# Kernel optimization log

Hardware: AMD Instinct MI355X
Metric: run time of the kernel (lower is better)

## Reference

```python
import jax, jax.numpy as jnp
import numpy as np

N_NODES = 100000
N_REL = 8
IN_FEATS = 64
ATTN_FEATS = 32
NUM_HEADS = 4
N_EDGES = 800000
NEG_SLOPE = 0.2


def setup_inputs() -> dict:
    key = jax.random.key(0)
    ks = jax.random.split(key, 11)
    s = 0.05
    return {
        "feat": jax.random.normal(ks[0], (N_NODES, IN_FEATS), jnp.float32),
        "quality_emb": jax.random.normal(ks[1], (N_NODES, IN_FEATS), jnp.float32),
        "fc_src_w": jax.random.normal(ks[2], (N_REL, IN_FEATS, ATTN_FEATS * NUM_HEADS), jnp.float32) * s,
        "fc_src_b": jax.random.normal(ks[3], (N_REL, ATTN_FEATS * NUM_HEADS), jnp.float32) * s,
        "fc_qual_w": jax.random.normal(ks[4], (N_REL, IN_FEATS, ATTN_FEATS * NUM_HEADS), jnp.float32) * s,
        "fc_qual_b": jax.random.normal(ks[5], (N_REL, ATTN_FEATS * NUM_HEADS), jnp.float32) * s,
        "attn": jax.random.normal(ks[6], (N_REL, NUM_HEADS, ATTN_FEATS), jnp.float32) * s,
        "src": jax.random.randint(ks[7], (N_EDGES,), 0, N_NODES, jnp.int64),
        "dst": jax.random.randint(ks[8], (N_EDGES,), 0, N_NODES, jnp.int64),
        "r_type": jax.random.randint(ks[9], (N_EDGES,), 0, N_REL, jnp.int64),
        "nid": jax.random.randint(ks[10], (N_EDGES,), 0, N_NODES, jnp.int64),
    }


def reference(feat, quality_emb, fc_src_w, fc_src_b, fc_qual_w, fc_qual_b, attn,
              src, dst, r_type, nid):
    # gather_mm(feat[src], fc_src_w, idx_b=r_type) == project per node for all
    # relations (grouped GEMM), then gather [src, r_type] per edge.
    feat_proj = jnp.einsum('ni,rio->nro', feat, fc_src_w)          # [N, R, H*D]
    el = feat_proj[src, r_type] + fc_src_b[r_type]                 # [E, H*D]

    qual_proj = jnp.einsum('ni,rio->nro', quality_emb, fc_qual_w)  # [N, R, H*D]
    qual = qual_proj[nid, r_type] + fc_qual_b[r_type]              # [E, H*D]

    e = jax.nn.leaky_relu((el + qual).reshape(-1, NUM_HEADS, ATTN_FEATS), NEG_SLOPE)
    score = jnp.sum(e * attn[r_type], axis=-1)                     # [E, H]

    # edge softmax grouped by destination node, per head
    m = jax.ops.segment_max(score, dst, num_segments=N_NODES)      # [N, H]
    p = jnp.exp(score - m[dst])
    denom = jax.ops.segment_sum(p, dst, num_segments=N_NODES)      # [N, H]
    a = p / denom[dst]                                             # [E, H]

    # narre: messages use raw source features, weighted by attention
    msg = feat[src][:, None, :] * a[:, :, None]                    # [E, H, IN]
    ft = jax.ops.segment_sum(msg, dst, num_segments=N_NODES)       # [N, H, IN]
    return ft
```

## Files before the change

### kernel.cpp

```cpp
#include <hip/hip_runtime.h>
#include <hip/hip_bf16.h>

#define RELS 8
#define HDD 128
#define NH 4
#define STILES 4

typedef __attribute__((ext_vector_type(8))) short bf16x8;
typedef __attribute__((ext_vector_type(4))) float f32x4;
typedef unsigned short u16;

__device__ __forceinline__ u16 f2b(float v){
  union { float f; unsigned u; } x; x.f = v;
  unsigned r = x.u + 0x7fffu + ((x.u >> 16) & 1u);
  return (u16)(r >> 16);
}
__device__ __forceinline__ float b2f(u16 h){
  union { unsigned u; float f; } x; x.u = ((unsigned)h) << 16; return x.f;
}

template<int CTRL>
__device__ __forceinline__ float dpp_mov(float x){
  union { float f; int i; } u; u.f = x;
  u.i = __builtin_amdgcn_update_dpp(0, u.i, CTRL, 0xF, 0xF, false);
  return u.f;
}
__device__ __forceinline__ float row_sum16(float v){
  v += dpp_mov<0x121>(v);
  v += dpp_mov<0x122>(v);
  v += dpp_mov<0x124>(v);
  v += dpp_mov<0x128>(v);
  return v;
}

__global__ void k_combo(const float* __restrict__ wsrc, const float* __restrict__ wqual,
                        const float* __restrict__ bsrc, const float* __restrict__ bqual,
                        u16* __restrict__ Wt, float* __restrict__ biasc,
                        const float* __restrict__ feat, const float* __restrict__ qual,
                        u16* __restrict__ featb, u16* __restrict__ qualb, int total,
                        const int* __restrict__ rt,
                        int* __restrict__ rcnt, int E,
                        int BH, int B0){
  int b = blockIdx.x, t = threadIdx.x;
  if (b < BH){
    __shared__ int lh[RELS];
    if (t < RELS) lh[t] = 0;
    __syncthreads();
    for (int e = b*256 + t; e < E; e += BH*256)
      atomicAdd(&lh[rt[e]], 1);
    __syncthreads();
    if (t < RELS && lh[t]) atomicAdd(&rcnt[t], lh[t]);
  } else if (b < BH + B0){
    int g = (b - BH)*256 + t;
    if (g < RELS*HDD*HDD){
      int r = g >> 14, rem = g & 16383, n = rem >> 7, k = rem & 127;
      float v = (k < 64) ? wsrc[r*8192 + k*128 + n] : wqual[r*8192 + (k-64)*128 + n];
      Wt[g] = f2b(v);
    } else {
      int bb = g - RELS*HDD*HDD;
      if (bb < RELS*HDD) biasc[bb] = bsrc[bb] + bqual[bb];
    }
  } else {
    int g = ((b - BH - B0)*256 + t) * 8;
    const float* sp; u16* dp;
    if (g < total){ sp = feat; dp = featb; }
    else { g -= total; if (g >= total) return; sp = qual; dp = qualb; }
    float4 a = *(const float4*)(sp + g);
    float4 c = *(const float4*)(sp + g + 4);
    union { u16 h[8]; uint4 v; } o;
    o.h[0]=f2b(a.x); o.h[1]=f2b(a.y); o.h[2]=f2b(a.z); o.h[3]=f2b(a.w);
    o.h[4]=f2b(c.x); o.h[5]=f2b(c.y); o.h[6]=f2b(c.z); o.h[7]=f2b(c.w);
    *(uint4*)(dp + g) = o.v;
  }
}

__global__ void k_scatter(const int* __restrict__ rt,
                          const int* __restrict__ src, const int* __restrict__ nid,
                          const int* __restrict__ dst,
                          const int* __restrict__ rcnt, int* __restrict__ rcur,
                          int* __restrict__ srcR, int* __restrict__ nidR,
                          int* __restrict__ dstR, int E){
  __shared__ int lh[RELS], lb[RELS];
  int t = threadIdx.x;
  if (t < RELS) lh[t] = 0;
  __syncthreads();
  int e = blockIdx.x*256 + t;
  int r = 0, rank = 0, sv = 0, nv = 0, dv = 0;
  if (e < E){
    sv = src[e]; nv = nid[e]; dv = dst[e];
    r = rt[e];
    rank = atomicAdd(&lh[r], 1);
  }
  __syncthreads();
  if (t < RELS){
    int ro = 0;
    #pragma unroll
    for (int i=0;i<RELS;i++) if (i < t) ro += rcnt[i];
    if (lh[t] > 0) lb[t] = ro + atomicAdd(&rcur[t], lh[t]);
  }
  __syncthreads();
  if (e < E){
    int pr = lb[r] + rank;
    srcR[pr] = sv;
    nidR[pr] = nv;
    dstR[pr] = dv;
  }
}

__global__ void k_scan_a(const int* __restrict__ deg, int* __restrict__ offD,
                         int* __restrict__ bsums, int N){
  __shared__ int s[256];
  int t = threadIdx.x, i = blockIdx.x*256 + t;
  int v = (i < N) ? deg[i] : 0;
  s[t] = v; __syncthreads();
  for (int off=1; off<256; off<<=1){
    int x = (t >= off) ? s[t-off] : 0;
    __syncthreads();
    s[t] += x;
    __syncthreads();
  }
  if (i < N) offD[i] = s[t] - v;
  if (t == 255) bsums[blockIdx.x] = s[255];
}

__global__ void k_scan_b(const int* __restrict__ bsums, int* __restrict__ bsums_sc,
                         int* __restrict__ offD, int NBLK, int N){
  __shared__ int s[512];
  int t = threadIdx.x;
  int v = (t < NBLK) ? bsums[t] : 0;
  s[t] = v; __syncthreads();
  for (int off=1; off<512; off<<=1){
    int x = (t >= off) ? s[t-off] : 0;
    __syncthreads();
    s[t] += x;
    __syncthreads();
  }
  if (t < NBLK) bsums_sc[t] = s[t] - v;
  if (t == NBLK-1) offD[N] = s[t];
}

__global__ void k_scan_c(int* __restrict__ offD, const int* __restrict__ bsums_sc, int N){
  int i = blockIdx.x*256 + threadIdx.x;
  if (i < N) offD[i] += bsums_sc[i >> 8];
}

__global__ __launch_bounds__(320) void k_score(
    const u16* __restrict__ featb, const u16* __restrict__ qualb,
    const u16* __restrict__ Wt, const float* __restrict__ biasc,
    const float* __restrict__ attn,
    const int* __restrict__ srcR, const int* __restrict__ nidR,
    const int* __restrict__ dstR, const int* __restrict__ rcnt,
    int* __restrict__ deg, int* __restrict__ rankR,
    float* __restrict__ scoreR, int E){
  __shared__ u16 As[2][64*128];
  int t = threadIdx.x;

  int bid = blockIdx.x;
  int r = -1, base = 0, cntR = 0;
  {
    int acc0 = 0, st = 0;
    #pragma unroll
    for (int rr=0; rr<RELS; rr++){
      int c = rcnt[rr];
      int nb = (c + 255) >> 8;
      if (r < 0 && bid < acc0 + nb){
        int ch = bid - acc0;
        r = rr; base = st + ch*256; cntR = min(256, c - ch*256);
      }
      acc0 += nb;
      st += c;
    }
  }
  if (r < 0) return;
  int Tact = (cntR + 63) >> 6;

  if (t >= 256){
    int hl = t - 256;
    int eh0=-1,eh1=-1,eh2=-1,eh3=-1;
    int rk0=0,rk1=0,rk2=0,rk3=0;
    if (hl < cntR)     { eh0 = base+hl;     rk0 = atomicAdd(&deg[dstR[eh0]],1); }
    if (64+hl < cntR)  { eh1 = base+64+hl;  rk1 = atomicAdd(&deg[dstR[eh1]],1); }
    if (128+hl < cntR) { eh2 = base+128+hl; rk2 = atomicAdd(&deg[dstR[eh2]],1); }
    if (192+hl < cntR) { eh3 = base+192+hl; rk3 = atomicAdd(&deg[dstR[eh3]],1); }
    for (int i=0;i<Tact;i++)
      __builtin_amdgcn_s_barrier();
    if (eh0>=0) rankR[eh0]=rk0;
    if (eh1>=0) rankR[eh1]=rk1;
    if (eh2>=0) rankR[eh2]=rk2;
    if (eh3>=0) rankR[eh3]=rk3;
    return;
  }

  int mloc = t >> 2, part = t & 3;
  int lane = t & 63, w = t >> 6;
  int lr = lane & 15, lq = lane >> 4;

  const u16* wbase = Wt + r*16384 + (w*32)*128;
  bf16x8 wfrag[2][4];
  #pragma unroll
  for (int mt=0; mt<2; mt++)
    #pragma unroll
    for (int kt=0; kt<4; kt++)
      wfrag[mt][kt] = *(const bf16x8*)(wbase + (mt*16 + lr)*128 + kt*32 + lq*8);

  float attn_p[2][4], attn_n[2][4];
  f32x4 biasv[2];
  #pragma unroll
  for (int mt=0; mt<2; mt++)
    #pragma unroll
    for (int i=0; i<4; i++){
      int c = w*32 + mt*16 + lq*4 + i;
      float a = attn[r*128 + c];
      biasv[mt][i] = biasc[r*128 + c];
      attn_p[mt][i] = a;
      attn_n[mt][i] = 0.2f*a;
    }

  const u16* basep = (part < 2) ? featb : qualb;
  int halfoff = (part & 1)*32;
  int myidx[STILES];
  #pragma unroll
  for (int tt=0; tt<STILES; tt++){
    int eloc = tt*64 + mloc;
    int gi = base + eloc;
    myidx[tt] = (eloc < cntR) ? ((part < 2) ? srcR[gi] : nidR[gi]) : -1;
  }

  uint4 pre[2][4];
  auto fetch = [&](int pb, int idxval){
    if (idxval >= 0){
      const uint4* pv = (const uint4*)(basep + (long long)idxval*64 + halfoff);
      pre[pb][0]=pv[0]; pre[pb][1]=pv[1]; pre[pb][2]=pv[2]; pre[pb][3]=pv[3];
    } else {
      uint4 z = {0,0,0,0};
      pre[pb][0]=z; pre[pb][1]=z; pre[pb][2]=z; pre[pb][3]=z;
    }
  };

  fetch(0, myidx[0]);
  fetch(1, myidx[1]);
  #pragma unroll
  for (int tt=0; tt<STILES; tt++){
    if (tt >= Tact) break;
    const int p = tt & 1;
    uint4* As_v = (uint4*)As[p];
    #pragma unroll
    for (int i=0;i<4;i++){
      int c = part*4 + i;
      As_v[mloc*16 + (c ^ part ^ (mloc & 7))] = pre[p][i];
    }
    if (tt+2 < STILES) fetch(p, myidx[tt+2]);
    asm volatile("s_waitcnt lgkmcnt(0)" ::: "memory");
    __builtin_amdgcn_s_barrier();

    f32x4 acc[4][2];
    #pragma unroll
    for (int et=0; et<4; et++){ acc[et][0]=biasv[0]; acc[et][1]=biasv[1]; }
    #pragma unroll
    for (int et=0; et<4; et++){
      #pragma unroll
      for (int kt=0; kt<4; kt++){
        bf16x8 bf = *(const bf16x8*)&As[p][(et*16 + lr)*128 + (((kt*4 + lq) ^ kt ^ (lr & 7))*8)];
        acc[et][0] = __builtin_amdgcn_mfma_f32_16x16x32_bf16(wfrag[0][kt], bf, acc[et][0], 0, 0, 0);
        acc[et][1] = __builtin_amdgcn_mfma_f32_16x16x32_bf16(wfrag[1][kt], bf, acc[et][1], 0, 0, 0);
      }
    }

    float s0v=0.f, s1v=0.f, s2v=0.f, s3v=0.f;
    #pragma unroll
    for (int mt=0; mt<2; mt++)
      #pragma unroll
      for (int i=0; i<4; i++){
        float x0 = acc[0][mt][i];
        s0v = __builtin_fmaf(fmaxf(x0,0.f), attn_p[mt][i], s0v);
        s0v = __builtin_fmaf(fminf(x0,0.f), attn_n[mt][i], s0v);
        float x1 = acc[1][mt][i];
        s1v = __builtin_fmaf(fmaxf(x1,0.f), attn_p[mt][i], s1v);
        s1v = __builtin_fmaf(fminf(x1,0.f), attn_n[mt][i], s1v);
        float x2 = acc[2][mt][i];
        s2v = __builtin_fmaf(fmaxf(x2,0.f), attn_p[mt][i], s2v);
        s2v = __builtin_fmaf(fminf(x2,0.f), attn_n[mt][i], s2v);
        float x3 = acc[3][mt][i];
        s3v = __builtin_fmaf(fmaxf(x3,0.f), attn_p[mt][i], s3v);
        s3v = __builtin_fmaf(fminf(x3,0.f), attn_n[mt][i], s3v);
      }
    s0v += __shfl_xor(s0v, 16); s0v += __shfl_xor(s0v, 32);
    s1v += __shfl_xor(s1v, 16); s1v += __shfl_xor(s1v, 32);
    s2v += __shfl_xor(s2v, 16); s2v += __shfl_xor(s2v, 32);
    s3v += __shfl_xor(s3v, 16); s3v += __shfl_xor(s3v, 32);
    float v01 = (lq & 1) ? s1v : s0v;
    float v23 = (lq & 1) ? s3v : s2v;
    float v = (lq & 2) ? v23 : v01;
    v = __expf(v);
    int eout = tt*64 + lane;
    if (eout < cntR) scoreR[(size_t)w*E + base + eout] = v;
  }
}

__global__ void k_perm(const int* __restrict__ dstR, const int* __restrict__ rankR,
                       const int* __restrict__ srcR, const float* __restrict__ scoreR,
                       const int* __restrict__ offD,
                       float* __restrict__ scoreD, int* __restrict__ srcD, int E){
  int pr = blockIdx.x*256 + threadIdx.x;
  if (pr >= E) return;
  int d = dstR[pr];
  int pd = offD[d] + rankR[pr];
  float4 sc;
  sc.x = scoreR[pr];
  sc.y = scoreR[(size_t)E + pr];
  sc.z = scoreR[(size_t)2*E + pr];
  sc.w = scoreR[(size_t)3*E + pr];
  *(float4*)&scoreD[(long long)pd*4] = sc;
  srcD[pd] = srcR[pr];
}

__global__ __launch_bounds__(256) void k_agg(
    const int* __restrict__ offD, const int* __restrict__ srcD,
    const float* __restrict__ scoreD,
    const u16* __restrict__ featb, float* __restrict__ out, int N){
  __shared__ float ps[4][64][4];
  __shared__ int   ss[4][64];
  int wv = threadIdx.x >> 6, lane = threadIdx.x & 63;
  int node = blockIdx.x*4 + wv;
  if (node >= N) return;
  int s0 = offD[node], s1 = offD[node+1];
  int deg = s1 - s0;
  float a0=0.f, a1=0.f, a2=0.f, a3=0.f;
  if (deg > 0){
    float d0=0.f,d1=0.f,d2=0.f,d3=0.f;
    for (int c=0; c<deg; c+=64){
      int j = c + lane;
      float p0=0.f,p1=0.f,p2=0.f,p3=0.f; int sv=0;
      if (j < deg){
        float4 sc = *(const float4*)&scoreD[(long long)(s0+j)*4];
        sv = srcD[s0+j];
        p0=sc.x; p1=sc.y; p2=sc.z; p3=sc.w;
      }
      d0+=p0; d1+=p1; d2+=p2; d3+=p3;
      float4 pv = { p0, p1, p2, p3 };
      *(float4*)&ps[wv][lane][0] = pv;
      ss[wv][lane] = sv;
      __builtin_amdgcn_wave_barrier();
      int cnt = min(64, deg - c);
      #pragma unroll 4
      for (int e=0; e<cnt; e++){
        float4 pe = *(const float4*)&ps[wv][e][0];
        float fv = b2f(featb[(long long)ss[wv][e]*64 + lane]);
        a0 += pe.x*fv; a1 += pe.y*fv; a2 += pe.z*fv; a3 += pe.w*fv;
      }
      __builtin_amdgcn_wave_barrier();
    }
    d0=row_sum16(d0); d1=row_sum16(d1); d2=row_sum16(d2); d3=row_sum16(d3);
    #pragma unroll
    for (int off=16; off<64; off<<=1){
      d0+=__shfl_xor(d0,off); d1+=__shfl_xor(d1,off);
      d2+=__shfl_xor(d2,off); d3+=__shfl_xor(d3,off);
    }
    a0 *= 1.f/d0; a1 *= 1.f/d1; a2 *= 1.f/d2; a3 *= 1.f/d3;
  }
  float* op = out + (long long)node*256;
  op[lane]       = a0;
  op[64 + lane]  = a1;
  op[128 + lane] = a2;
  op[192 + lane] = a3;
}

extern "C" void kernel_launch(void* const* d_in, const int* in_sizes, int n_in,
                              void* d_out, int out_size, void* d_ws, size_t ws_size,
                              hipStream_t stream) {
  const float* feat  = (const float*)d_in[0];
  const float* qual  = (const float*)d_in[1];
  const float* wsrc  = (const float*)d_in[2];
  const float* bsrc  = (const float*)d_in[3];
  const float* wqual = (const float*)d_in[4];
  const float* bqual = (const float*)d_in[5];
  const float* attn  = (const float*)d_in[6];
  const int* src = (const int*)d_in[7];
  const int* dst = (const int*)d_in[8];
  const int* rt  = (const int*)d_in[9];
  const int* nid = (const int*)d_in[10];
  const int E = in_sizes[7];
  const int N = in_sizes[0] / 64;
  float* out = (float*)d_out;

  char* p = (char*)d_ws;
  auto alloc = [&](size_t bytes) -> void* {
    void* q = (void*)p;
    p += (bytes + 255) & ~(size_t)255;
    return q;
  };
  float* scoreD  = (float*)alloc((size_t)E*4*4);
  float* scoreR  = (float*)alloc((size_t)E*4*4);
  u16*  featb    = (u16*)  alloc((size_t)N*64*2);
  u16*  qualb    = (u16*)  alloc((size_t)N*64*2);
  u16*  Wt       = (u16*)  alloc((size_t)RELS*HDD*HDD*2);
  float* biasc   = (float*)alloc((size_t)RELS*HDD*4);
  int*  srcD     = (int*)  alloc((size_t)E*4);
  int*  srcR     = (int*)  alloc((size_t)E*4);
  int*  nidR     = (int*)  alloc((size_t)E*4);
  int*  dstR     = (int*)  alloc((size_t)E*4);
  int*  rankR    = (int*)  alloc((size_t)E*4);
  int*  offD     = (int*)  alloc((size_t)(N+1)*4);
  int*  bsums    = (int*)  alloc(4096);
  int*  bsums_sc = (int*)  alloc(4096);
  char* zbase = p;
  int*  deg      = (int*)  alloc((size_t)N*4);
  int*  rcnt     = (int*)  alloc(32);
  int*  rcur     = (int*)  alloc(32);
  size_t zbytes = (size_t)(p - zbase);

  hipMemsetAsync(zbase, 0, zbytes, stream);

  int total = N*64;
  int totw = RELS*HDD*HDD + RELS*HDD;
  int BH = 512;
  int B0 = (totw + 255)/256;
  int B1 = ((2*total)/8 + 255)/256;
  int B2 = (E + 255)/256;
  k_combo<<<BH+B0+B1, 256, 0, stream>>>(wsrc, wqual, bsrc, bqual, Wt, biasc,
                                        feat, qual, featb, qualb, total,
                                        rt, rcnt, E, BH, B0);
  k_scatter<<<B2, 256, 0, stream>>>(rt, src, nid, dst, rcnt, rcur,
                                    srcR, nidR, dstR, E);
  int NBS = B2 + RELS;
  k_score<<<NBS, 320, 0, stream>>>(featb, qualb, Wt, biasc, attn,
                                   srcR, nidR, dstR, rcnt, deg, rankR, scoreR, E);
  int NBLK = (N + 255)/256;
  k_scan_a<<<NBLK, 256, 0, stream>>>(deg, offD, bsums, N);
  k_scan_b<<<1, 512, 0, stream>>>(bsums, bsums_sc, offD, NBLK, N);
  k_scan_c<<<NBLK, 256, 0, stream>>>(offD, bsums_sc, N);
  k_perm<<<B2, 256, 0, stream>>>(dstR, rankR, srcR, scoreR, offD, scoreD, srcD, E);
  k_agg<<<(N + 3)/4, 256, 0, stream>>>(offD, srcD, scoreD, featb, out, N);
}
```

Before: 370.1 us.

## Move degree counting into scatter and fuse permutation into score kernel

Destination-degree atomics and rank computation move from extra warps in the score kernel into the relation scatter kernel. The scan now runs before scoring, so the score kernel can write scores and source ids directly into destination-sorted order. This removes the separate permutation kernel and the intermediate relation-ordered score buffer. In exchange the score kernel does scattered 4-byte stores per head instead of a coalesced write, and it loses the overlap between the degree atomics and the MFMA work.

```diff
diff --git a/kernel.cpp b/kernel.cpp
--- a/kernel.cpp
+++ b/kernel.cpp
@@ -78,16 +78,18 @@
                           const int* __restrict__ src, const int* __restrict__ nid,
                           const int* __restrict__ dst,
                           const int* __restrict__ rcnt, int* __restrict__ rcur,
+                          int* __restrict__ deg,
                           int* __restrict__ srcR, int* __restrict__ nidR,
-                          int* __restrict__ dstR, int E){
+                          int* __restrict__ dstR, int* __restrict__ rankR, int E){
   __shared__ int lh[RELS], lb[RELS];
   int t = threadIdx.x;
   if (t < RELS) lh[t] = 0;
   __syncthreads();
   int e = blockIdx.x*256 + t;
-  int r = 0, rank = 0, sv = 0, nv = 0, dv = 0;
+  int r = 0, rank = 0, sv = 0, nv = 0, dv = 0, rk = 0;
   if (e < E){
     sv = src[e]; nv = nid[e]; dv = dst[e];
+    rk = atomicAdd(&deg[dv], 1);
     r = rt[e];
     rank = atomicAdd(&lh[r], 1);
   }
@@ -104,6 +106,7 @@
     srcR[pr] = sv;
     nidR[pr] = nv;
     dstR[pr] = dv;
+    rankR[pr] = rk;
   }
 }
 
@@ -144,15 +147,17 @@
   if (i < N) offD[i] += bsums_sc[i >> 8];
 }
 
-__global__ __launch_bounds__(320) void k_score(
+__global__ __launch_bounds__(256) void k_score(
     const u16* __restrict__ featb, const u16* __restrict__ qualb,
     const u16* __restrict__ Wt, const float* __restrict__ biasc,
     const float* __restrict__ attn,
     const int* __restrict__ srcR, const int* __restrict__ nidR,
-    const int* __restrict__ dstR, const int* __restrict__ rcnt,
-    int* __restrict__ deg, int* __restrict__ rankR,
-    float* __restrict__ scoreR, int E){
+    const int* __restrict__ dstR, const int* __restrict__ rankR,
+    const int* __restrict__ rcnt, const int* __restrict__ offD,
+    int* __restrict__ srcD,
+    float* __restrict__ scoreD){
   __shared__ u16 As[2][64*128];
+  __shared__ int pos_s[2][64];
   int t = threadIdx.x;
 
   int bid = blockIdx.x;
@@ -174,23 +179,6 @@
   if (r < 0) return;
   int Tact = (cntR + 63) >> 6;
 
-  if (t >= 256){
-    int hl = t - 256;
-    int eh0=-1,eh1=-1,eh2=-1,eh3=-1;
-    int rk0=0,rk1=0,rk2=0,rk3=0;
-    if (hl < cntR)     { eh0 = base+hl;     rk0 = atomicAdd(&deg[dstR[eh0]],1); }
-    if (64+hl < cntR)  { eh1 = base+64+hl;  rk1 = atomicAdd(&deg[dstR[eh1]],1); }
-    if (128+hl < cntR) { eh2 = base+128+hl; rk2 = atomicAdd(&deg[dstR[eh2]],1); }
-    if (192+hl < cntR) { eh3 = base+192+hl; rk3 = atomicAdd(&deg[dstR[eh3]],1); }
-    for (int i=0;i<Tact;i++)
-      __builtin_amdgcn_s_barrier();
-    if (eh0>=0) rankR[eh0]=rk0;
-    if (eh1>=0) rankR[eh1]=rk1;
-    if (eh2>=0) rankR[eh2]=rk2;
-    if (eh3>=0) rankR[eh3]=rk3;
-    return;
-  }
-
   int mloc = t >> 2, part = t & 3;
   int lane = t & 63, w = t >> 6;
   int lr = lane & 15, lq = lane >> 4;
@@ -218,12 +206,19 @@
 
   const u16* basep = (part < 2) ? featb : qualb;
   int halfoff = (part & 1)*32;
-  int myidx[STILES];
+  int myidx[STILES], mypos[STILES];
   #pragma unroll
   for (int tt=0; tt<STILES; tt++){
     int eloc = tt*64 + mloc;
+    bool v = (eloc < cntR);
     int gi = base + eloc;
-    myidx[tt] = (eloc < cntR) ? ((part < 2) ? srcR[gi] : nidR[gi]) : -1;
+    myidx[tt] = v ? ((part < 2) ? srcR[gi] : nidR[gi]) : -1;
+    mypos[tt] = -1;
+    if (part == 0 && v){
+      int pd = offD[dstR[gi]] + rankR[gi];
+      mypos[tt] = pd;
+      srcD[pd] = myidx[tt];
+    }
   }
 
   uint4 pre[2][4];
@@ -249,9 +244,9 @@
       int c = part*4 + i;
       As_v[mloc*16 + (c ^ part ^ (mloc & 7))] = pre[p][i];
     }
+    if (part == 0) pos_s[p][mloc] = mypos[tt];
     if (tt+2 < STILES) fetch(p, myidx[tt+2]);
-    asm volatile("s_waitcnt lgkmcnt(0)" ::: "memory");
-    __builtin_amdgcn_s_barrier();
+    __syncthreads();
 
     f32x4 acc[4][2];
     #pragma unroll
@@ -292,26 +287,9 @@
     float v23 = (lq & 1) ? s3v : s2v;
     float v = (lq & 2) ? v23 : v01;
     v = __expf(v);
-    int eout = tt*64 + lane;
-    if (eout < cntR) scoreR[(size_t)w*E + base + eout] = v;
-  }
-}
-
-__global__ void k_perm(const int* __restrict__ dstR, const int* __restrict__ rankR,
-                       const int* __restrict__ srcR, const float* __restrict__ scoreR,
-                       const int* __restrict__ offD,
-                       float* __restrict__ scoreD, int* __restrict__ srcD, int E){
-  int pr = blockIdx.x*256 + threadIdx.x;
-  if (pr >= E) return;
-  int d = dstR[pr];
-  int pd = offD[d] + rankR[pr];
-  float4 sc;
-  sc.x = scoreR[pr];
-  sc.y = scoreR[(size_t)E + pr];
-  sc.z = scoreR[(size_t)2*E + pr];
-  sc.w = scoreR[(size_t)3*E + pr];
-  *(float4*)&scoreD[(long long)pd*4] = sc;
-  srcD[pd] = srcR[pr];
+    int pd = pos_s[p][lane];
+    if (pd >= 0) scoreD[(long long)pd*4 + w] = v;
+  }
 }
 
 __global__ __launch_bounds__(256) void k_agg(
@@ -390,7 +368,6 @@
     return q;
   };
   float* scoreD  = (float*)alloc((size_t)E*4*4);
-  float* scoreR  = (float*)alloc((size_t)E*4*4);
   u16*  featb    = (u16*)  alloc((size_t)N*64*2);
   u16*  qualb    = (u16*)  alloc((size_t)N*64*2);
   u16*  Wt       = (u16*)  alloc((size_t)RELS*HDD*HDD*2);
@@ -420,15 +397,15 @@
   k_combo<<<BH+B0+B1, 256, 0, stream>>>(wsrc, wqual, bsrc, bqual, Wt, biasc,
                                         feat, qual, featb, qualb, total,
                                         rt, rcnt, E, BH, B0);
-  k_scatter<<<B2, 256, 0, stream>>>(rt, src, nid, dst, rcnt, rcur,
-                                    srcR, nidR, dstR, E);
-  int NBS = B2 + RELS;
-  k_score<<<NBS, 320, 0, stream>>>(featb, qualb, Wt, biasc, attn,
-                                   srcR, nidR, dstR, rcnt, deg, rankR, scoreR, E);
+  k_scatter<<<B2, 256, 0, stream>>>(rt, src, nid, dst, rcnt, rcur, deg,
+                                    srcR, nidR, dstR, rankR, E);
   int NBLK = (N + 255)/256;
   k_scan_a<<<NBLK, 256, 0, stream>>>(deg, offD, bsums, N);
   k_scan_b<<<1, 512, 0, stream>>>(bsums, bsums_sc, offD, NBLK, N);
   k_scan_c<<<NBLK, 256, 0, stream>>>(offD, bsums_sc, N);
-  k_perm<<<B2, 256, 0, stream>>>(dstR, rankR, srcR, scoreR, offD, scoreD, srcD, E);
+  int NBS = B2 + RELS;
+  k_score<<<NBS, 256, 0, stream>>>(featb, qualb, Wt, biasc, attn,
+                                   srcR, nidR, dstR, rankR, rcnt, offD,
+                                   srcD, scoreD);
   k_agg<<<(N + 3)/4, 256, 0, stream>>>(offD, srcD, scoreD, featb, out, N);
 }
```

New measurement: 335.7 us. 9.3% less time.

## Move degree histogram into dedicated blocks and pad degree counters

Applied to the files above, without the earlier changes.

The per-edge atomic degree counting moves out of the extra 64-thread wave in each score block and into 256 dedicated leading blocks that grid-stride over edges with four loads and atomics in flight per thread. Score blocks drop to 256 threads and no longer run the barrier-matching loop for the histogram wave. Each degree counter is padded to 16 ints so that concurrent atomics on different nodes do not hit the same cache line. The cost is a 16x larger zeroed degree array and strided reads in the scan.

```diff
diff --git a/kernel.cpp b/kernel.cpp
--- a/kernel.cpp
+++ b/kernel.cpp
@@ -5,6 +5,8 @@
 #define HDD 128
 #define NH 4
 #define STILES 4
+#define DEGS 16
+#define BHIST 256
 
 typedef __attribute__((ext_vector_type(8))) short bf16x8;
 typedef __attribute__((ext_vector_type(4))) float f32x4;
@@ -111,7 +113,7 @@
                          int* __restrict__ bsums, int N){
   __shared__ int s[256];
   int t = threadIdx.x, i = blockIdx.x*256 + t;
-  int v = (i < N) ? deg[i] : 0;
+  int v = (i < N) ? deg[(size_t)i*DEGS] : 0;
   s[t] = v; __syncthreads();
   for (int off=1; off<256; off<<=1){
     int x = (t >= off) ? s[t-off] : 0;
@@ -144,7 +146,7 @@
   if (i < N) offD[i] += bsums_sc[i >> 8];
 }
 
-__global__ __launch_bounds__(320) void k_score(
+__global__ __launch_bounds__(256) void k_score(
     const u16* __restrict__ featb, const u16* __restrict__ qualb,
     const u16* __restrict__ Wt, const float* __restrict__ biasc,
     const float* __restrict__ attn,
@@ -154,8 +156,25 @@
     float* __restrict__ scoreR, int E){
   __shared__ u16 As[2][64*128];
   int t = threadIdx.x;
-
-  int bid = blockIdx.x;
+  int b = blockIdx.x;
+
+  if (b < BHIST){
+    const int stride = BHIST*256;
+    for (int pr0 = b*256 + t; pr0 < E; pr0 += 4*stride){
+      int prs[4], dvs[4], rks[4];
+      #pragma unroll
+      for (int u=0;u<4;u++) prs[u] = pr0 + u*stride;
+      #pragma unroll
+      for (int u=0;u<4;u++) if (prs[u] < E) dvs[u] = dstR[prs[u]];
+      #pragma unroll
+      for (int u=0;u<4;u++) if (prs[u] < E) rks[u] = atomicAdd(&deg[(size_t)dvs[u]*DEGS], 1);
+      #pragma unroll
+      for (int u=0;u<4;u++) if (prs[u] < E) rankR[prs[u]] = rks[u];
+    }
+    return;
+  }
+
+  int bid = b - BHIST;
   int r = -1, base = 0, cntR = 0;
   {
     int acc0 = 0, st = 0;
@@ -173,23 +192,6 @@
   }
   if (r < 0) return;
   int Tact = (cntR + 63) >> 6;
-
-  if (t >= 256){
-    int hl = t - 256;
-    int eh0=-1,eh1=-1,eh2=-1,eh3=-1;
-    int rk0=0,rk1=0,rk2=0,rk3=0;
-    if (hl < cntR)     { eh0 = base+hl;     rk0 = atomicAdd(&deg[dstR[eh0]],1); }
-    if (64+hl < cntR)  { eh1 = base+64+hl;  rk1 = atomicAdd(&deg[dstR[eh1]],1); }
-    if (128+hl < cntR) { eh2 = base+128+hl; rk2 = atomicAdd(&deg[dstR[eh2]],1); }
-    if (192+hl < cntR) { eh3 = base+192+hl; rk3 = atomicAdd(&deg[dstR[eh3]],1); }
-    for (int i=0;i<Tact;i++)
-      __builtin_amdgcn_s_barrier();
-    if (eh0>=0) rankR[eh0]=rk0;
-    if (eh1>=0) rankR[eh1]=rk1;
-    if (eh2>=0) rankR[eh2]=rk2;
-    if (eh3>=0) rankR[eh3]=rk3;
-    return;
-  }
 
   int mloc = t >> 2, part = t & 3;
   int lane = t & 63, w = t >> 6;
@@ -404,7 +406,7 @@
   int*  bsums    = (int*)  alloc(4096);
   int*  bsums_sc = (int*)  alloc(4096);
   char* zbase = p;
-  int*  deg      = (int*)  alloc((size_t)N*4);
+  int*  deg      = (int*)  alloc((size_t)N*DEGS*4);
   int*  rcnt     = (int*)  alloc(32);
   int*  rcur     = (int*)  alloc(32);
   size_t zbytes = (size_t)(p - zbase);
@@ -423,8 +425,9 @@
   k_scatter<<<B2, 256, 0, stream>>>(rt, src, nid, dst, rcnt, rcur,
                                     srcR, nidR, dstR, E);
   int NBS = B2 + RELS;
-  k_score<<<NBS, 320, 0, stream>>>(featb, qualb, Wt, biasc, attn,
-                                   srcR, nidR, dstR, rcnt, deg, rankR, scoreR, E);
+  k_score<<<BHIST + NBS, 256, 0, stream>>>(featb, qualb, Wt, biasc, attn,
+                                           srcR, nidR, dstR, rcnt,
+                                           deg, rankR, scoreR, E);
   int NBLK = (N + 255)/256;
   k_scan_a<<<NBLK, 256, 0, stream>>>(deg, offD, bsums, N);
   k_scan_b<<<1, 512, 0, stream>>>(bsums, bsums_sc, offD, NBLK, N);
```

After: 351.4 us. 5.1% less time.
